# Kernel tuning notes

Hardware: AMD Instinct MI355X
Metric: run time of the kernel (lower is better)

The kernel has to match this reference:

```python
import jax, jax.numpy as jnp
import numpy as np

B, N, HIST, PRED = 32, 1500, 24, 24
OUT, FDIM = 1, 31
IN = OUT + FDIM          # 32 = chebconv in_dim
HID, GCN, K, E = 256, 256, 3, 24000


def setup_inputs() -> dict:
    key = jax.random.key(0)
    ks = jax.random.split(key, 8)
    x_hist = jax.random.normal(ks[0], (B, HIST, N, OUT), jnp.float32)
    features = jax.random.normal(ks[1], (B, HIST + PRED, N, FDIM), jnp.float32)
    edge_index = jax.random.randint(ks[2], (2, E), 0, N, dtype=jnp.int32)
    s_cheb = 1.0 / np.sqrt(IN)
    s_ih = 1.0 / np.sqrt(HID)
    W_cheb = jax.random.normal(ks[3], (K, IN, GCN), jnp.float32) * s_cheb
    b_cheb = jnp.zeros((GCN,), jnp.float32)
    W_ih = jax.random.normal(ks[4], (3 * HID, IN + GCN), jnp.float32) * s_ih
    b_ih = jnp.zeros((3 * HID,), jnp.float32)
    W_hh = jax.random.normal(ks[5], (3 * HID, HID), jnp.float32) * s_ih
    b_hh = jnp.zeros((3 * HID,), jnp.float32)
    W_fc = jax.random.normal(ks[6], (OUT, HID), jnp.float32) * s_ih
    b_fc = jnp.zeros((OUT,), jnp.float32)
    return dict(x_hist=x_hist, features=features, edge_index=edge_index,
                W_cheb=W_cheb, b_cheb=b_cheb, W_ih=W_ih, b_ih=b_ih,
                W_hh=W_hh, b_hh=b_hh, W_fc=W_fc, b_fc=b_fc)


def _edge_norm(edge_index):
    # sym-normalized Laplacian scaled by 2/lambda_max with lambda_max=2:
    # L_hat = -D^{-1/2} A D^{-1/2} (zero diagonal)
    src, dst = edge_index[0], edge_index[1]
    deg = jax.ops.segment_sum(jnp.ones((E,), jnp.float32), src, num_segments=N)
    dis = jnp.where(deg > 0, jax.lax.rsqrt(jnp.maximum(deg, 1.0)), 0.0)
    w = -(dis[src] * dis[dst])
    return src, dst, w


def _cheb(x, src, dst, w, W_cheb, b_cheb):
    # x: [B, N, D]; Chebyshev recursion Tx_k = 2 L_hat Tx_{k-1} - Tx_{k-2}
    def Lx(v):
        msg = v[:, src, :] * w[None, :, None]          # [B, E, D]
        return jnp.zeros_like(v).at[:, dst, :].add(msg)
    Tx0 = x
    out = jnp.einsum('bnd,df->bnf', Tx0, W_cheb[0])
    Tx1 = Lx(x)
    out = out + jnp.einsum('bnd,df->bnf', Tx1, W_cheb[1])
    for k in range(2, W_cheb.shape[0]):
        Tx2 = 2.0 * Lx(Tx1) - Tx0
        out = out + jnp.einsum('bnd,df->bnf', Tx2, W_cheb[k])
        Tx0, Tx1 = Tx1, Tx2
    return out + b_cheb


def _gru(x, h, W_ih, b_ih, W_hh, b_hh):
    # x: [B*N, IN+GCN], h: [B*N, HID]; torch.nn.GRUCell math
    gi = x @ W_ih.T + b_ih
    gh = h @ W_hh.T + b_hh
    i_r, i_z, i_n = jnp.split(gi, 3, axis=-1)
    h_r, h_z, h_n = jnp.split(gh, 3, axis=-1)
    r = jax.nn.sigmoid(i_r + h_r)
    z = jax.nn.sigmoid(i_z + h_z)
    n = jnp.tanh(i_n + r * h_n)
    return (1.0 - z) * n + z * h


def reference(x_hist, features, edge_index, W_cheb, b_cheb, W_ih, b_ih, W_hh, b_hh, W_fc, b_fc):
    src, dst, w = _edge_norm(edge_index)

    def step(h, x_t):
        g = jax.nn.sigmoid(_cheb(x_t, src, dst, w, W_cheb, b_cheb))   # [B,N,GCN]
        xg = jnp.concatenate([x_t, g], axis=-1).reshape(B * N, IN + GCN)
        return _gru(xg, h, W_ih, b_ih, W_hh, b_hh)

    # encoder: t = 1 .. hist_len-1, x_t = [x_hist[:,t-1], features[:,t]]
    xs = jnp.concatenate([x_hist[:, :HIST - 1], features[:, 1:HIST]], axis=-1)
    xs = jnp.moveaxis(xs, 1, 0)                                       # [HIST-1,B,N,IN]
    h0 = jnp.zeros((B * N, HID), x_hist.dtype)
    hn, _ = jax.lax.scan(lambda h, x_t: (step(h, x_t), None), h0, xs)

    feats_dec = jnp.moveaxis(features[:, HIST:], 1, 0)                # [PRED,B,N,FDIM]

    def dec_step(carry, f_t):
        h, x_prev = carry
        x_t = jnp.concatenate([x_prev, f_t], axis=-1)                 # [B,N,IN]
        h = step(h, x_t)
        x_new = h.reshape(B, N, HID) @ W_fc.T + b_fc                  # [B,N,OUT]
        return (h, x_new), x_new

    (_, _), ys = jax.lax.scan(dec_step, (hn, x_hist[:, -1]), feats_dec)
    return jnp.moveaxis(ys, 0, 1)                                     # [B,PRED,N,OUT]
```

## Files before the change

kernel.cpp:

```cpp
#include <hip/hip_runtime.h>
#include <hip/hip_bf16.h>
#include <math.h>

#define NB 32
#define NN 1500
#define NE 24000
#define HIST_L 24
#define PRED_L 24
#define FDIM 31
#define INUM 32
#define HID 256
#define ROWS (NB*NN)
#define XGW 320
#define CTXW 96
#define NRB 375

typedef float f32x4 __attribute__((ext_vector_type(4)));
typedef short bf16x8 __attribute__((ext_vector_type(8)));
typedef short bf16x4 __attribute__((ext_vector_type(4)));

__device__ __forceinline__ float sigf(float x){ return 1.0f/(1.0f+expf(-x)); }
__device__ __forceinline__ unsigned short f2b(float f){
    __hip_bfloat16 h = __float2bfloat16(f);
    return __builtin_bit_cast(unsigned short, h);
}
__device__ __forceinline__ float b2f(unsigned short u){
    unsigned int x = ((unsigned int)u) << 16;
    return __builtin_bit_cast(float, x);
}

#define AS1 __attribute__((address_space(1)))
#define AS3 __attribute__((address_space(3)))
__device__ __forceinline__ void gload16(const void* g, void* l){
    __builtin_amdgcn_global_load_lds((const AS1 unsigned int*)g, (AS3 unsigned int*)l, 16, 0, 0);
}

__global__ void k_count(const int* __restrict__ ei, int* deg, int* cnt){
    int e = blockIdx.x*blockDim.x + threadIdx.x;
    if (e < NE){ atomicAdd(&deg[ei[e]], 1); atomicAdd(&cnt[ei[NE+e]], 1); }
}

__global__ void k_prefix(const int* __restrict__ cnt, int* __restrict__ coff){
    int lane = threadIdx.x;
    const int CH = (NN + 63)/64;
    int s = 0;
    for (int i=0;i<CH;i++){ int n = lane*CH+i; if (n<NN) s += cnt[n]; }
    int incl = s;
    for (int off=1; off<64; off<<=1){ int v = __shfl_up(incl, off); if (lane>=off) incl += v; }
    int run = incl - s;
    for (int i=0;i<CH;i++){ int n = lane*CH+i; if (n<NN){ coff[n] = run; run += cnt[n]; } }
    if (lane==63) coff[NN] = run;
}

__global__ __launch_bounds__(256) void k_fillw(
    const int* __restrict__ ei, const int* __restrict__ deg,
    const int* __restrict__ coff, int* __restrict__ csrc, float* __restrict__ cw){
    int n = blockIdx.x*4 + (threadIdx.x >> 6);
    if (n >= NN) return;
    int lane = threadIdx.x & 63;
    int dn = deg[n];
    float disn = dn>0 ? rsqrtf((float)dn) : 0.0f;
    int pos = coff[n];
    for (int base=0; base<NE; base+=64){
        int e = base + lane;
        int d = ei[NE+e];
        bool m = (d == n);
        unsigned long long mask = __ballot(m);
        if (m){
            int rank = __popcll(mask & ((1ull<<lane)-1ull));
            int s = ei[e];
            int ds = deg[s];
            float diss = ds>0 ? rsqrtf((float)ds) : 0.0f;
            csrc[pos+rank] = s;
            cw[pos+rank] = -(diss*disn);
        }
        pos += __popcll(mask);
    }
}

__global__ void k_f2b(const float* __restrict__ src, unsigned short* __restrict__ dst, int n){
    int i = blockIdx.x*256 + threadIdx.x;
    if (i < n) dst[i] = f2b(src[i]);
}
__global__ void k_wihr(const float* __restrict__ W, unsigned short* __restrict__ Wr){
    int i = blockIdx.x*256 + threadIdx.x;
    if (i < 768*XGW){
        int r = i/XGW, c = i - r*XGW;
        Wr[i] = (c < INUM+HID) ? f2b(W[(size_t)r*(INUM+HID) + c]) : (unsigned short)0;
    }
}
__global__ void k_wctr(const float* __restrict__ Wc, unsigned short* __restrict__ W){
    int i = blockIdx.x*256 + threadIdx.x;
    if (i < 256*96){
        int j = i/96, k = i - j*96;
        W[i] = f2b(Wc[(size_t)k*256 + j]);
    }
}

__global__ void k_build(const float* __restrict__ ch0, int bstride, int choff0, int chstep, int addb,
                        const float* __restrict__ bfc,
                        const float* __restrict__ feats, int tf0,
                        float* __restrict__ xt, unsigned short* __restrict__ ctx,
                        unsigned short* __restrict__ xg){
    int s = blockIdx.y;
    int idx = blockIdx.x*blockDim.x + threadIdx.x;
    if (idx >= ROWS*INUM) return;
    xt  += (size_t)s*ROWS*INUM;
    ctx += (size_t)s*ROWS*CTXW;
    xg  += (size_t)s*ROWS*XGW;
    int choff = choff0 + s*chstep;
    int tf = tf0 + s;
    int r = idx >> 5, c = idx & 31;
    int b = r / NN, n = r - b*NN;
    float v;
    if (c == 0){ v = ch0[b*bstride + choff + n]; if (addb) v += bfc[0]; }
    else         v = feats[((size_t)(b*(HIST_L+PRED_L) + tf)*NN + n)*FDIM + (c-1)];
    xt[idx] = v;
    unsigned short bv = f2b(v);
    ctx[(size_t)r*CTXW + c] = bv;
    xg[(size_t)r*XGW + c] = bv;
}

__global__ void k_lx4(const float* __restrict__ vin, const int* __restrict__ coff,
                      const int* __restrict__ csrc, const float* __restrict__ cw,
                      const float* __restrict__ sub, float scale,
                      float* __restrict__ vout, unsigned short* __restrict__ ctxo){
    int s = blockIdx.y;
    int idx = blockIdx.x*256 + threadIdx.x;
    if (idx >= ROWS*8) return;
    vin += (size_t)s*ROWS*INUM;
    if (sub)  sub  += (size_t)s*ROWS*INUM;
    if (vout) vout += (size_t)s*ROWS*INUM;
    ctxo += (size_t)s*ROWS*CTXW;
    int r = idx >> 3, l8 = idx & 7;
    int b = r / NN, n = r - b*NN;
    int j0 = coff[n], j1 = coff[n+1];
    const float4* vb = (const float4*)(vin + (size_t)b*NN*INUM);
    float ax=0.f, ay=0.f, az=0.f, aw=0.f;
    for (int j=j0;j<j1;j++){
        float w = cw[j];
        float4 v = vb[csrc[j]*8 + l8];
        ax += w*v.x; ay += w*v.y; az += w*v.z; aw += w*v.w;
    }
    ax *= scale; ay *= scale; az *= scale; aw *= scale;
    if (sub){
        float4 sv = ((const float4*)sub)[idx];
        ax -= sv.x; ay -= sv.y; az -= sv.z; aw -= sv.w;
    }
    if (vout){
        float4 o; o.x=ax; o.y=ay; o.z=az; o.w=aw;
        ((float4*)vout)[idx] = o;
    }
    bf16x4 ob;
    ob[0]=(short)f2b(ax); ob[1]=(short)f2b(ay); ob[2]=(short)f2b(az); ob[3]=(short)f2b(aw);
    *(bf16x4*)&ctxo[(size_t)r*CTXW + l8*4] = ob;
}

__global__ __launch_bounds__(256,2) void k_cheb3(
    const unsigned short* __restrict__ ctx, const unsigned short* __restrict__ Wctr,
    const float* __restrict__ bc, unsigned short* __restrict__ xg)
{
    __shared__ __align__(16) unsigned short A[128*104];
    __shared__ __align__(16) unsigned short B[256*104];
    const int bi = blockIdx.x;
    const int s = bi / NRB, rb = bi - s*NRB;
    ctx += (size_t)s*ROWS*CTXW;
    xg  += (size_t)s*ROWS*XGW;
    const int tid = threadIdx.x, wid = tid>>6, lane = tid&63;
    const int wm = wid>>1, wn = wid&1;
    const int r0 = rb*128;
    const int l15 = lane&15, lhi = lane>>4;

    #pragma unroll
    for (int i=0;i<6;i++){
        int idx = tid + i*256;
        int row = idx/12, c = idx - row*12;
        *(int4*)&A[row*104 + c*8] = *(const int4*)&ctx[(size_t)(r0+row)*96 + c*8];
    }
    #pragma unroll
    for (int i=0;i<12;i++){
        int idx = tid + i*256;
        int row = idx/12, c = idx - row*12;
        *(int4*)&B[row*104 + c*8] = *(const int4*)&Wctr[(size_t)row*96 + c*8];
    }
    __syncthreads();

    f32x4 acc[4][8] = {};
    #pragma unroll
    for (int ks=0; ks<3; ks++){
        bf16x8 a[4];
        #pragma unroll
        for (int mi=0;mi<4;mi++)
            a[mi] = *(const bf16x8*)&A[(wm*64+mi*16+l15)*104 + ks*32 + lhi*8];
        #pragma unroll
        for (int ni=0;ni<8;ni++){
            bf16x8 b = *(const bf16x8*)&B[(wn*128+ni*16+l15)*104 + ks*32 + lhi*8];
            #pragma unroll
            for (int mi=0;mi<4;mi++)
                acc[mi][ni] = __builtin_amdgcn_mfma_f32_16x16x32_bf16(a[mi], b, acc[mi][ni],0,0,0);
        }
    }
    #pragma unroll
    for (int ni=0;ni<8;ni++){
        int col = wn*128 + ni*16 + l15;
        float bcv = bc[col];
        #pragma unroll
        for (int mi=0;mi<4;mi++){
            #pragma unroll
            for (int v=0;v<4;v++){
                size_t row = r0 + wm*64 + mi*16 + lhi*4 + v;
                xg[row*XGW + 32 + col] = f2b(sigf(acc[mi][ni][v] + bcv));
            }
        }
    }
}

__device__ __forceinline__ void gtile32(const unsigned short* Ap, const unsigned short* Bp,
    int wm, int wn, int l15, int q,
    f32x4 (&ar)[4][2], f32x4 (&az)[4][2], f32x4 (&a3)[4][2])
{
    bf16x8 a[4];
    #pragma unroll
    for (int mi=0;mi<4;mi++)
        a[mi] = *(const bf16x8*)&Ap[(wm*64 + mi*16 + l15)*32 + q];
    #pragma unroll
    for (int slab=0; slab<3; slab++){
        bf16x8 b0 = *(const bf16x8*)&Bp[(slab*64 + wn*32 + l15)*32 + q];
        bf16x8 b1 = *(const bf16x8*)&Bp[(slab*64 + wn*32 + 16 + l15)*32 + q];
        f32x4 (&acc)[4][2] = (slab==0)?ar:((slab==1)?az:a3);
        #pragma unroll
        for (int mi=0;mi<4;mi++){
            acc[mi][0] = __builtin_amdgcn_mfma_f32_16x16x32_bf16(a[mi], b0, acc[mi][0],0,0,0);
            acc[mi][1] = __builtin_amdgcn_mfma_f32_16x16x32_bf16(a[mi], b1, acc[mi][1],0,0,0);
        }
    }
}

__global__ __launch_bounds__(256,2) void k_gru6(
    const unsigned short* __restrict__ xg, const unsigned short* __restrict__ hbin,
    const unsigned short* __restrict__ Wihr, const unsigned short* __restrict__ Whhr,
    const float* __restrict__ bih, const float* __restrict__ bhh,
    unsigned short* __restrict__ hbout,
    const float* __restrict__ Wfc, float* __restrict__ outp, int p)
{
    __shared__ __align__(16) unsigned short As[2][128*32];
    __shared__ __align__(16) unsigned short Bs[2][192*32];
    const int bi = blockIdx.x;
    const int xc = bi & 7, t = bi >> 3;
    const int R = xc + 8*(t>>2);
    if (R >= NRB) return;
    const int r0 = R*128, j0 = (t&3)*64;

    const int tid = threadIdx.x, wid = tid>>6, lane = tid&63;
    const int wm = wid>>1, wn = wid&1;
    const int l15 = lane&15, lhi = lane>>4;
    const int r4 = lane>>2;
    const int swz = ((lane&3) ^ ((lane>>3)&3))*16;
    const int q   = (lhi ^ ((l15>>1)&3))*8;

    f32x4 ar[4][2]={}, az[4][2]={}, ain[4][2]={}, ahn[4][2]={};

    auto stageA = [&](int ks, int bs){
        const char* src; size_t stride;
        if (ks < 9){ src = (const char*)xg   + (size_t)r0*640 + (size_t)ks*64;     stride = 640; }
        else       { src = (const char*)hbin + (size_t)r0*512 + (size_t)(ks-9)*64; stride = 512; }
        char* Ld = (char*)&As[bs][0] + wid*2048;
        #pragma unroll
        for (int i=0;i<2;i++){
            int lrow = wid*32 + i*16 + r4;
            gload16(src + (size_t)lrow*stride + swz, Ld + i*1024);
        }
    };
    auto stageB = [&](int ks, int bs){
        const char* src; size_t stride; int kb;
        if (ks < 9){ src = (const char*)Wihr; stride = 640; kb = ks; }
        else       { src = (const char*)Whhr; stride = 512; kb = ks-9; }
        src += (size_t)kb*64 + swz;
        char* Ld = (char*)&Bs[bs][0] + wid*3072;
        #pragma unroll
        for (int i=0;i<3;i++){
            int j = wid*3 + i;
            int wrow = (j>>2)*256 + j0 + (j&3)*16 + r4;
            gload16(src + (size_t)wrow*stride, Ld + i*1024);
        }
    };

    stageA(0,0); stageB(0,0);
    __syncthreads();
    for (int ks=0; ks<9; ks++){
        int cur = ks&1;
        { stageA(ks+1, cur^1); stageB(ks+1, cur^1); }
        gtile32(&As[cur][0], &Bs[cur][0], wm, wn, l15, q, ar, az, ain);
        __syncthreads();
    }
    for (int ks=9; ks<17; ks++){
        int cur = ks&1;
        if (ks<16){ stageA(ks+1, cur^1); stageB(ks+1, cur^1); }
        gtile32(&As[cur][0], &Bs[cur][0], wm, wn, l15, q, ar, az, ahn);
        __syncthreads();
    }
    float fcp[4][4] = {};
    float wf[2];
    if (p >= 0){
        wf[0] = Wfc[j0 + wn*32 + l15];
        wf[1] = Wfc[j0 + wn*32 + 16 + l15];
    }
    #pragma unroll
    for (int ni=0; ni<2; ni++){
        int col = j0 + wn*32 + ni*16 + l15;
        float br = bih[col]       + bhh[col];
        float bz = bih[col+HID]   + bhh[col+HID];
        float bi2 = bih[col+2*HID];
        float bh = bhh[col+2*HID];
        #pragma unroll
        for (int mi=0; mi<4; mi++){
            #pragma unroll
            for (int v=0; v<4; v++){
                size_t row = r0 + wm*64 + mi*16 + lhi*4 + v;
                float r  = sigf(ar[mi][ni][v] + br);
                float z  = sigf(az[mi][ni][v] + bz);
                float nn = tanhf(ain[mi][ni][v] + bi2 + r*(ahn[mi][ni][v] + bh));
                float ho = b2f(hbin[row*HID + col]);
                float hv = (1.f - z)*nn + z*ho;
                hbout[row*HID + col] = f2b(hv);
                if (p >= 0) fcp[mi][v] += hv * wf[ni];
            }
        }
    }
    if (p >= 0){
        #pragma unroll
        for (int mi=0; mi<4; mi++){
            #pragma unroll
            for (int v=0; v<4; v++){
                float s = fcp[mi][v];
                s += __shfl_xor(s, 1);
                s += __shfl_xor(s, 2);
                s += __shfl_xor(s, 4);
                s += __shfl_xor(s, 8);
                if (l15 == 0){
                    int row = r0 + wm*64 + mi*16 + lhi*4 + v;
                    int bb = row / NN, n = row - bb*NN;
                    atomicAdd(&outp[(size_t)(bb*PRED_L + p)*NN + n], s);
                }
            }
        }
    }
}

extern "C" void kernel_launch(void* const* d_in, const int* in_sizes, int n_in,
                              void* d_out, int out_size, void* d_ws, size_t ws_size,
                              hipStream_t stream){
    const float* x_hist = (const float*)d_in[0];
    const float* feats  = (const float*)d_in[1];
    const int*   ei     = (const int*)d_in[2];
    const float* Wc     = (const float*)d_in[3];
    const float* bc     = (const float*)d_in[4];
    const float* Wih    = (const float*)d_in[5];
    const float* bih    = (const float*)d_in[6];
    const float* Whh    = (const float*)d_in[7];
    const float* bhh    = (const float*)d_in[8];
    const float* Wfc    = (const float*)d_in[9];
    const float* bfc    = (const float*)d_in[10];
    float* out = (float*)d_out;

    char* wsp = (char*)d_ws;
    size_t off = 0;
    auto alloc = [&](size_t bytes)->char*{
        char* p = wsp + off; off = (off + bytes + 255) & ~(size_t)255; return p;
    };
    int*   deg  = (int*)  alloc(NN*4);
    int*   cnt  = (int*)  alloc(NN*4);
    int*   coff = (int*)  alloc((NN+1)*4);
    int*   csrc = (int*)  alloc(NE*4);
    float* cw   = (float*)alloc(NE*4);
    unsigned short* hbA = (unsigned short*)alloc((size_t)ROWS*HID*2);
    unsigned short* hbB = (unsigned short*)alloc((size_t)ROWS*HID*2);
    unsigned short* Wihr = (unsigned short*)alloc((size_t)768*XGW*2);
    unsigned short* Whhr = (unsigned short*)alloc((size_t)768*HID*2);
    unsigned short* Wctr = (unsigned short*)alloc((size_t)256*CTXW*2);

    const size_t perSlice = (size_t)ROWS*INUM*4*2 + (size_t)ROWS*CTXW*2 + (size_t)ROWS*XGW*2 + 4*256;
    int CH = 1;
    for (int c : {8,6,4,2}){
        if (off + (size_t)c*perSlice + (1<<20) <= ws_size){ CH = c; break; }
    }
    float* xt_b = (float*)alloc((size_t)CH*ROWS*INUM*4);
    float* T1_b = (float*)alloc((size_t)CH*ROWS*INUM*4);
    unsigned short* ctx_b = (unsigned short*)alloc((size_t)CH*ROWS*CTXW*2);
    unsigned short* xg_b  = (unsigned short*)alloc((size_t)CH*ROWS*XGW*2);

    hipMemsetAsync(deg, 0, NN*4, stream);
    hipMemsetAsync(cnt, 0, NN*4, stream);
    hipMemsetAsync(hbA, 0, (size_t)ROWS*HID*2, stream);
    hipMemsetAsync(xg_b, 0, (size_t)CH*ROWS*XGW*2, stream);
    hipMemsetAsync(out, 0, (size_t)out_size*4, stream);

    k_count<<<(NE+255)/256,256,0,stream>>>(ei, deg, cnt);
    k_prefix<<<1,64,0,stream>>>(cnt, coff);
    k_fillw<<<NRB,256,0,stream>>>(ei, deg, coff, csrc, cw);

    { int n = 768*XGW; k_wihr<<<(n+255)/256,256,0,stream>>>(Wih, Wihr); }
    { int n = 768*HID; k_f2b<<<(n+255)/256,256,0,stream>>>(Whh, Whhr, n); }
    { int n = 256*CTXW; k_wctr<<<(n+255)/256,256,0,stream>>>(Wc, Wctr); }

    unsigned short* hbin = hbA; unsigned short* hbout = hbB;
    const int gruGrid = 1504;
    const int NT  = (ROWS*INUM+255)/256;
    const int NT8 = (ROWS*8+255)/256;

    for (int t0=0; t0<HIST_L-1; t0+=CH){
        int nc = HIST_L-1-t0; if (nc > CH) nc = CH;
        dim3 gb(NT, nc), gl(NT8, nc);
        k_build<<<gb,256,0,stream>>>(x_hist, HIST_L*NN, t0*NN, NN, 0, bfc, feats, t0+1, xt_b, ctx_b, xg_b);
        k_lx4<<<gl,256,0,stream>>>(xt_b, coff, csrc, cw, nullptr, 1.f, T1_b, ctx_b + 32);
        k_lx4<<<gl,256,0,stream>>>(T1_b, coff, csrc, cw, xt_b, 2.f, nullptr, ctx_b + 64);
        k_cheb3<<<NRB*nc,256,0,stream>>>(ctx_b, Wctr, bc, xg_b);
        for (int s=0; s<nc; s++){
            k_gru6<<<gruGrid,256,0,stream>>>(xg_b + (size_t)s*ROWS*XGW, hbin, Wihr, Whhr, bih, bhh, hbout, Wfc, out, -1);
            unsigned short* tmp = hbin; hbin = hbout; hbout = tmp;
        }
    }
    for (int p=0;p<PRED_L;p++){
        dim3 gb(NT,1), gl(NT8,1);
        if (p==0) k_build<<<gb,256,0,stream>>>(x_hist, HIST_L*NN, (HIST_L-1)*NN, 0, 0, bfc, feats, HIST_L+p, xt_b, ctx_b, xg_b);
        else      k_build<<<gb,256,0,stream>>>(out, PRED_L*NN, (p-1)*NN, 0, 1, bfc, feats, HIST_L+p, xt_b, ctx_b, xg_b);
        k_lx4<<<gl,256,0,stream>>>(xt_b, coff, csrc, cw, nullptr, 1.f, T1_b, ctx_b + 32);
        k_lx4<<<gl,256,0,stream>>>(T1_b, coff, csrc, cw, xt_b, 2.f, nullptr, ctx_b + 64);
        k_cheb3<<<NRB,256,0,stream>>>(ctx_b, Wctr, bc, xg_b);
        k_gru6<<<gruGrid,256,0,stream>>>(xg_b, hbin, Wihr, Whhr, bih, bhh, hbout, Wfc, out, p);
        unsigned short* tmp = hbin; hbin = hbout; hbout = tmp;
    }
}
```

Baseline: 6.928 ms.

## Fuse recurrent GRU and decoder steps into one persistent cooperative kernel

The encoder's Chebyshev inputs for all 23 timesteps are now precomputed in chunks into one large xg buffer. A single cooperative persistent kernel then runs every encoder GRU step and every full decoder step, with grid.sync between phases. The GRU, Chebyshev matmul and graph-propagation phases become grid-stride device functions sharing one static LDS block. This aims to remove about 150 kernel launches and their gaps, in exchange for grid-wide barrier costs, a much larger workspace, and a GRU tile order that loses the previous L2-friendly block swizzle.

```diff
diff --git a/kernel.cpp b/kernel.cpp
--- a/kernel.cpp
+++ b/kernel.cpp
@@ -1,6 +1,9 @@
 #include <hip/hip_runtime.h>
 #include <hip/hip_bf16.h>
+#include <hip/hip_cooperative_groups.h>
 #include <math.h>
+
+namespace cg = cooperative_groups;
 
 #define NB 32
 #define NN 1500
@@ -236,21 +239,13 @@
     }
 }
 
-__global__ __launch_bounds__(256,2) void k_gru6(
+__device__ __forceinline__ void gru_phase(char* smem,
     const unsigned short* __restrict__ xg, const unsigned short* __restrict__ hbin,
+    unsigned short* __restrict__ hbout,
     const unsigned short* __restrict__ Wihr, const unsigned short* __restrict__ Whhr,
     const float* __restrict__ bih, const float* __restrict__ bhh,
-    unsigned short* __restrict__ hbout,
     const float* __restrict__ Wfc, float* __restrict__ outp, int p)
 {
-    __shared__ __align__(16) unsigned short As[2][128*32];
-    __shared__ __align__(16) unsigned short Bs[2][192*32];
-    const int bi = blockIdx.x;
-    const int xc = bi & 7, t = bi >> 3;
-    const int R = xc + 8*(t>>2);
-    if (R >= NRB) return;
-    const int r0 = R*128, j0 = (t&3)*64;
-
     const int tid = threadIdx.x, wid = tid>>6, lane = tid&63;
     const int wm = wid>>1, wn = wid&1;
     const int l15 = lane&15, lhi = lane>>4;
@@ -258,92 +253,237 @@
     const int swz = ((lane&3) ^ ((lane>>3)&3))*16;
     const int q   = (lhi ^ ((l15>>1)&3))*8;
 
-    f32x4 ar[4][2]={}, az[4][2]={}, ain[4][2]={}, ahn[4][2]={};
-
-    auto stageA = [&](int ks, int bs){
-        const char* src; size_t stride;
-        if (ks < 9){ src = (const char*)xg   + (size_t)r0*640 + (size_t)ks*64;     stride = 640; }
-        else       { src = (const char*)hbin + (size_t)r0*512 + (size_t)(ks-9)*64; stride = 512; }
-        char* Ld = (char*)&As[bs][0] + wid*2048;
-        #pragma unroll
-        for (int i=0;i<2;i++){
-            int lrow = wid*32 + i*16 + r4;
-            gload16(src + (size_t)lrow*stride + swz, Ld + i*1024);
-        }
-    };
-    auto stageB = [&](int ks, int bs){
-        const char* src; size_t stride; int kb;
-        if (ks < 9){ src = (const char*)Wihr; stride = 640; kb = ks; }
-        else       { src = (const char*)Whhr; stride = 512; kb = ks-9; }
-        src += (size_t)kb*64 + swz;
-        char* Ld = (char*)&Bs[bs][0] + wid*3072;
-        #pragma unroll
-        for (int i=0;i<3;i++){
-            int j = wid*3 + i;
-            int wrow = (j>>2)*256 + j0 + (j&3)*16 + r4;
-            gload16(src + (size_t)wrow*stride, Ld + i*1024);
-        }
-    };
-
-    stageA(0,0); stageB(0,0);
-    __syncthreads();
-    for (int ks=0; ks<9; ks++){
-        int cur = ks&1;
-        { stageA(ks+1, cur^1); stageB(ks+1, cur^1); }
-        gtile32(&As[cur][0], &Bs[cur][0], wm, wn, l15, q, ar, az, ain);
+    for (int job = blockIdx.x; job < NRB*4; job += gridDim.x){
+        const int r0 = (job>>2)*128, j0 = (job&3)*64;
+        f32x4 ar[4][2]={}, az[4][2]={}, ain[4][2]={}, ahn[4][2]={};
+
+        auto stageA = [&](int ks, int bs){
+            const char* src; size_t stride;
+            if (ks < 9){ src = (const char*)xg   + (size_t)r0*640 + (size_t)ks*64;     stride = 640; }
+            else       { src = (const char*)hbin + (size_t)r0*512 + (size_t)(ks-9)*64; stride = 512; }
+            char* Ld = smem + bs*8192 + wid*2048;
+            #pragma unroll
+            for (int i=0;i<2;i++){
+                int lrow = wid*32 + i*16 + r4;
+                gload16(src + (size_t)lrow*stride + swz, Ld + i*1024);
+            }
+        };
+        auto stageB = [&](int ks, int bs){
+            const char* src; size_t stride; int kb;
+            if (ks < 9){ src = (const char*)Wihr; stride = 640; kb = ks; }
+            else       { src = (const char*)Whhr; stride = 512; kb = ks-9; }
+            src += (size_t)kb*64 + swz;
+            char* Ld = smem + 16384 + bs*12288 + wid*3072;
+            #pragma unroll
+            for (int i=0;i<3;i++){
+                int j = wid*3 + i;
+                int wrow = (j>>2)*256 + j0 + (j&3)*16 + r4;
+                gload16(src + (size_t)wrow*stride, Ld + i*1024);
+            }
+        };
+
+        stageA(0,0); stageB(0,0);
         __syncthreads();
-    }
-    for (int ks=9; ks<17; ks++){
-        int cur = ks&1;
-        if (ks<16){ stageA(ks+1, cur^1); stageB(ks+1, cur^1); }
-        gtile32(&As[cur][0], &Bs[cur][0], wm, wn, l15, q, ar, az, ahn);
+        for (int ks=0; ks<9; ks++){
+            int cur = ks&1;
+            stageA(ks+1, cur^1); stageB(ks+1, cur^1);
+            gtile32((const unsigned short*)(smem + cur*8192),
+                    (const unsigned short*)(smem + 16384 + cur*12288), wm, wn, l15, q, ar, az, ain);
+            __syncthreads();
+        }
+        for (int ks=9; ks<17; ks++){
+            int cur = ks&1;
+            if (ks<16){ stageA(ks+1, cur^1); stageB(ks+1, cur^1); }
+            gtile32((const unsigned short*)(smem + cur*8192),
+                    (const unsigned short*)(smem + 16384 + cur*12288), wm, wn, l15, q, ar, az, ahn);
+            __syncthreads();
+        }
+        float fcp[4][4] = {};
+        float wf[2];
+        if (p >= 0){
+            wf[0] = Wfc[j0 + wn*32 + l15];
+            wf[1] = Wfc[j0 + wn*32 + 16 + l15];
+        }
+        #pragma unroll
+        for (int ni=0; ni<2; ni++){
+            int col = j0 + wn*32 + ni*16 + l15;
+            float br = bih[col]       + bhh[col];
+            float bz = bih[col+HID]   + bhh[col+HID];
+            float bi2 = bih[col+2*HID];
+            float bh = bhh[col+2*HID];
+            #pragma unroll
+            for (int mi=0; mi<4; mi++){
+                #pragma unroll
+                for (int v=0; v<4; v++){
+                    size_t row = r0 + wm*64 + mi*16 + lhi*4 + v;
+                    float r  = sigf(ar[mi][ni][v] + br);
+                    float z  = sigf(az[mi][ni][v] + bz);
+                    float nn = tanhf(ain[mi][ni][v] + bi2 + r*(ahn[mi][ni][v] + bh));
+                    float ho = b2f(hbin[row*HID + col]);
+                    float hv = (1.f - z)*nn + z*ho;
+                    hbout[row*HID + col] = f2b(hv);
+                    if (p >= 0) fcp[mi][v] += hv * wf[ni];
+                }
+            }
+        }
+        if (p >= 0){
+            #pragma unroll
+            for (int mi=0; mi<4; mi++){
+                #pragma unroll
+                for (int v=0; v<4; v++){
+                    float s = fcp[mi][v];
+                    s += __shfl_xor(s, 1);
+                    s += __shfl_xor(s, 2);
+                    s += __shfl_xor(s, 4);
+                    s += __shfl_xor(s, 8);
+                    if (l15 == 0){
+                        int row = r0 + wm*64 + mi*16 + lhi*4 + v;
+                        int bb = row / NN, n = row - bb*NN;
+                        atomicAdd(&outp[(size_t)(bb*PRED_L + p)*NN + n], s);
+                    }
+                }
+            }
+        }
+    }
+}
+
+__device__ __forceinline__ void cheb_phase(char* smem,
+    const unsigned short* __restrict__ ctx, const unsigned short* __restrict__ Wctr,
+    const float* __restrict__ bc, unsigned short* __restrict__ xg)
+{
+    unsigned short* A = (unsigned short*)smem;
+    unsigned short* B = (unsigned short*)(smem + 26624);
+    const int tid = threadIdx.x, wid = tid>>6, lane = tid&63;
+    const int wm = wid>>1, wn = wid&1;
+    const int l15 = lane&15, lhi = lane>>4;
+    for (int jb = blockIdx.x; jb < NRB; jb += gridDim.x){
+        const int r0 = jb*128;
+        #pragma unroll
+        for (int i=0;i<6;i++){
+            int idx = tid + i*256;
+            int row = idx/12, c = idx - row*12;
+            *(int4*)&A[row*104 + c*8] = *(const int4*)&ctx[(size_t)(r0+row)*96 + c*8];
+        }
+        #pragma unroll
+        for (int i=0;i<12;i++){
+            int idx = tid + i*256;
+            int row = idx/12, c = idx - row*12;
+            *(int4*)&B[row*104 + c*8] = *(const int4*)&Wctr[(size_t)row*96 + c*8];
+        }
         __syncthreads();
-    }
-    float fcp[4][4] = {};
-    float wf[2];
-    if (p >= 0){
-        wf[0] = Wfc[j0 + wn*32 + l15];
-        wf[1] = Wfc[j0 + wn*32 + 16 + l15];
-    }
-    #pragma unroll
-    for (int ni=0; ni<2; ni++){
-        int col = j0 + wn*32 + ni*16 + l15;
-        float br = bih[col]       + bhh[col];
-        float bz = bih[col+HID]   + bhh[col+HID];
-        float bi2 = bih[col+2*HID];
-        float bh = bhh[col+2*HID];
-        #pragma unroll
-        for (int mi=0; mi<4; mi++){
-            #pragma unroll
-            for (int v=0; v<4; v++){
-                size_t row = r0 + wm*64 + mi*16 + lhi*4 + v;
-                float r  = sigf(ar[mi][ni][v] + br);
-                float z  = sigf(az[mi][ni][v] + bz);
-                float nn = tanhf(ain[mi][ni][v] + bi2 + r*(ahn[mi][ni][v] + bh));
-                float ho = b2f(hbin[row*HID + col]);
-                float hv = (1.f - z)*nn + z*ho;
-                hbout[row*HID + col] = f2b(hv);
-                if (p >= 0) fcp[mi][v] += hv * wf[ni];
-            }
-        }
-    }
-    if (p >= 0){
-        #pragma unroll
-        for (int mi=0; mi<4; mi++){
-            #pragma unroll
-            for (int v=0; v<4; v++){
-                float s = fcp[mi][v];
-                s += __shfl_xor(s, 1);
-                s += __shfl_xor(s, 2);
-                s += __shfl_xor(s, 4);
-                s += __shfl_xor(s, 8);
-                if (l15 == 0){
-                    int row = r0 + wm*64 + mi*16 + lhi*4 + v;
-                    int bb = row / NN, n = row - bb*NN;
-                    atomicAdd(&outp[(size_t)(bb*PRED_L + p)*NN + n], s);
+        f32x4 acc[4][8] = {};
+        #pragma unroll
+        for (int ks=0; ks<3; ks++){
+            bf16x8 a[4];
+            #pragma unroll
+            for (int mi=0;mi<4;mi++)
+                a[mi] = *(const bf16x8*)&A[(wm*64+mi*16+l15)*104 + ks*32 + lhi*8];
+            #pragma unroll
+            for (int ni=0;ni<8;ni++){
+                bf16x8 b = *(const bf16x8*)&B[(wn*128+ni*16+l15)*104 + ks*32 + lhi*8];
+                #pragma unroll
+                for (int mi=0;mi<4;mi++)
+                    acc[mi][ni] = __builtin_amdgcn_mfma_f32_16x16x32_bf16(a[mi], b, acc[mi][ni],0,0,0);
+            }
+        }
+        #pragma unroll
+        for (int ni=0;ni<8;ni++){
+            int col = wn*128 + ni*16 + l15;
+            float bcv = bc[col];
+            #pragma unroll
+            for (int mi=0;mi<4;mi++){
+                #pragma unroll
+                for (int v=0;v<4;v++){
+                    size_t row = r0 + wm*64 + mi*16 + lhi*4 + v;
+                    xg[row*XGW + 32 + col] = f2b(sigf(acc[mi][ni][v] + bcv));
                 }
             }
         }
+        __syncthreads();
+    }
+}
+
+__device__ __forceinline__ void lx_phase(
+    const float* __restrict__ vin, const int* __restrict__ coff,
+    const int* __restrict__ csrc, const float* __restrict__ cw,
+    const float* __restrict__ sub, float scale,
+    float* __restrict__ vout, unsigned short* __restrict__ ctxo)
+{
+    const int stride = gridDim.x*blockDim.x;
+    for (int idx = blockIdx.x*blockDim.x + threadIdx.x; idx < ROWS*8; idx += stride){
+        int r = idx >> 3, l8 = idx & 7;
+        int b = r / NN, n = r - b*NN;
+        int j0 = coff[n], j1 = coff[n+1];
+        const float4* vb = (const float4*)(vin + (size_t)b*NN*INUM);
+        float ax=0.f, ay=0.f, az=0.f, aw=0.f;
+        for (int j=j0;j<j1;j++){
+            float w = cw[j];
+            float4 v = vb[csrc[j]*8 + l8];
+            ax += w*v.x; ay += w*v.y; az += w*v.z; aw += w*v.w;
+        }
+        ax *= scale; ay *= scale; az *= scale; aw *= scale;
+        if (sub){
+            float4 sv = ((const float4*)sub)[idx];
+            ax -= sv.x; ay -= sv.y; az -= sv.z; aw -= sv.w;
+        }
+        if (vout){
+            float4 o; o.x=ax; o.y=ay; o.z=az; o.w=aw;
+            ((float4*)vout)[idx] = o;
+        }
+        bf16x4 ob;
+        ob[0]=(short)f2b(ax); ob[1]=(short)f2b(ay); ob[2]=(short)f2b(az); ob[3]=(short)f2b(aw);
+        *(bf16x4*)&ctxo[(size_t)r*CTXW + l8*4] = ob;
+    }
+}
+
+__global__ __launch_bounds__(256,2) void k_recur(
+    unsigned short* xg_b, float* xt, float* T1, unsigned short* ctx,
+    unsigned short* hbA, unsigned short* hbB,
+    const unsigned short* Wihr, const unsigned short* Whhr, const unsigned short* Wctr,
+    const float* bih, const float* bhh, const float* bc, const float* bfc,
+    const float* Wfc, const float* x_hist, const float* feats,
+    const int* coff, const int* csrc, const float* cw, float* out)
+{
+    cg::grid_group grid = cg::this_grid();
+    __shared__ __align__(16) char smem[79872];
+    unsigned short* hbin = hbA;
+    unsigned short* hbout = hbB;
+    const int gstride = gridDim.x*blockDim.x;
+
+    for (int t=0; t<HIST_L-1; ++t){
+        gru_phase(smem, xg_b + (size_t)t*ROWS*XGW, hbin, hbout, Wihr, Whhr, bih, bhh, Wfc, out, -1);
+        { unsigned short* tmp=hbin; hbin=hbout; hbout=tmp; }
+        grid.sync();
+    }
+    for (int p=0; p<PRED_L; ++p){
+        {
+            const float* ch0 = (p==0)? x_hist : out;
+            const int bstride = (p==0)? HIST_L*NN : PRED_L*NN;
+            const int choff = (p==0)? (HIST_L-1)*NN : (p-1)*NN;
+            const int addb = (p==0)? 0 : 1;
+            const int tf = HIST_L + p;
+            for (int idx = blockIdx.x*blockDim.x + threadIdx.x; idx < ROWS*INUM; idx += gstride){
+                int r = idx >> 5, c = idx & 31;
+                int b = r / NN, n = r - b*NN;
+                float v;
+                if (c == 0){ v = ch0[b*bstride + choff + n]; if (addb) v += bfc[0]; }
+                else         v = feats[((size_t)(b*(HIST_L+PRED_L) + tf)*NN + n)*FDIM + (c-1)];
+                xt[idx] = v;
+                unsigned short bv = f2b(v);
+                ctx[(size_t)r*CTXW + c] = bv;
+                xg_b[(size_t)r*XGW + c] = bv;
+            }
+        }
+        grid.sync();
+        lx_phase(xt, coff, csrc, cw, nullptr, 1.f, T1, ctx + 32);
+        grid.sync();
+        lx_phase(T1, coff, csrc, cw, xt, 2.f, nullptr, ctx + 64);
+        grid.sync();
+        cheb_phase(smem, ctx, Wctr, bc, xg_b);
+        grid.sync();
+        gru_phase(smem, xg_b, hbin, hbout, Wihr, Whhr, bih, bhh, Wfc, out, p);
+        { unsigned short* tmp=hbin; hbin=hbout; hbout=tmp; }
+        grid.sync();
     }
 }
 
@@ -379,7 +519,9 @@
     unsigned short* Whhr = (unsigned short*)alloc((size_t)768*HID*2);
     unsigned short* Wctr = (unsigned short*)alloc((size_t)256*CTXW*2);
 
-    const size_t perSlice = (size_t)ROWS*INUM*4*2 + (size_t)ROWS*CTXW*2 + (size_t)ROWS*XGW*2 + 4*256;
+    unsigned short* xg_b = (unsigned short*)alloc((size_t)(HIST_L-1)*ROWS*XGW*2);
+
+    const size_t perSlice = (size_t)ROWS*INUM*4*2 + (size_t)ROWS*CTXW*2 + 4*256;
     int CH = 1;
     for (int c : {8,6,4,2}){
         if (off + (size_t)c*perSlice + (1<<20) <= ws_size){ CH = c; break; }
@@ -387,12 +529,11 @@
     float* xt_b = (float*)alloc((size_t)CH*ROWS*INUM*4);
     float* T1_b = (float*)alloc((size_t)CH*ROWS*INUM*4);
     unsigned short* ctx_b = (unsigned short*)alloc((size_t)CH*ROWS*CTXW*2);
-    unsigned short* xg_b  = (unsigned short*)alloc((size_t)CH*ROWS*XGW*2);
 
     hipMemsetAsync(deg, 0, NN*4, stream);
     hipMemsetAsync(cnt, 0, NN*4, stream);
     hipMemsetAsync(hbA, 0, (size_t)ROWS*HID*2, stream);
-    hipMemsetAsync(xg_b, 0, (size_t)CH*ROWS*XGW*2, stream);
+    hipMemsetAsync(xg_b, 0, (size_t)(HIST_L-1)*ROWS*XGW*2, stream);
     hipMemsetAsync(out, 0, (size_t)out_size*4, stream);
 
     k_count<<<(NE+255)/256,256,0,stream>>>(ei, deg, cnt);
@@ -403,31 +544,32 @@
     { int n = 768*HID; k_f2b<<<(n+255)/256,256,0,stream>>>(Whh, Whhr, n); }
     { int n = 256*CTXW; k_wctr<<<(n+255)/256,256,0,stream>>>(Wc, Wctr); }
 
-    unsigned short* hbin = hbA; unsigned short* hbout = hbB;
-    const int gruGrid = 1504;
     const int NT  = (ROWS*INUM+255)/256;
     const int NT8 = (ROWS*8+255)/256;
 
     for (int t0=0; t0<HIST_L-1; t0+=CH){
         int nc = HIST_L-1-t0; if (nc > CH) nc = CH;
         dim3 gb(NT, nc), gl(NT8, nc);
-        k_build<<<gb,256,0,stream>>>(x_hist, HIST_L*NN, t0*NN, NN, 0, bfc, feats, t0+1, xt_b, ctx_b, xg_b);
+        unsigned short* xg_t = xg_b + (size_t)t0*ROWS*XGW;
+        k_build<<<gb,256,0,stream>>>(x_hist, HIST_L*NN, t0*NN, NN, 0, bfc, feats, t0+1, xt_b, ctx_b, xg_t);
         k_lx4<<<gl,256,0,stream>>>(xt_b, coff, csrc, cw, nullptr, 1.f, T1_b, ctx_b + 32);
         k_lx4<<<gl,256,0,stream>>>(T1_b, coff, csrc, cw, xt_b, 2.f, nullptr, ctx_b + 64);
-        k_cheb3<<<NRB*nc,256,0,stream>>>(ctx_b, Wctr, bc, xg_b);
-        for (int s=0; s<nc; s++){
-            k_gru6<<<gruGrid,256,0,stream>>>(xg_b + (size_t)s*ROWS*XGW, hbin, Wihr, Whhr, bih, bhh, hbout, Wfc, out, -1);
-            unsigned short* tmp = hbin; hbin = hbout; hbout = tmp;
-        }
-    }
-    for (int p=0;p<PRED_L;p++){
-        dim3 gb(NT,1), gl(NT8,1);
-        if (p==0) k_build<<<gb,256,0,stream>>>(x_hist, HIST_L*NN, (HIST_L-1)*NN, 0, 0, bfc, feats, HIST_L+p, xt_b, ctx_b, xg_b);
-        else      k_build<<<gb,256,0,stream>>>(out, PRED_L*NN, (p-1)*NN, 0, 1, bfc, feats, HIST_L+p, xt_b, ctx_b, xg_b);
-        k_lx4<<<gl,256,0,stream>>>(xt_b, coff, csrc, cw, nullptr, 1.f, T1_b, ctx_b + 32);
-        k_lx4<<<gl,256,0,stream>>>(T1_b, coff, csrc, cw, xt_b, 2.f, nullptr, ctx_b + 64);
-        k_cheb3<<<NRB,256,0,stream>>>(ctx_b, Wctr, bc, xg_b);
-        k_gru6<<<gruGrid,256,0,stream>>>(xg_b, hbin, Wihr, Whhr, bih, bhh, hbout, Wfc, out, p);
-        unsigned short* tmp = hbin; hbin = hbout; hbout = tmp;
-    }
-}
+        k_cheb3<<<NRB*nc,256,0,stream>>>(ctx_b, Wctr, bc, xg_t);
+    }
+
+    int maxb = 0;
+    if (hipOccupancyMaxActiveBlocksPerMultiprocessor(&maxb, (const void*)k_recur, 256, 0) != hipSuccess || maxb < 1)
+        maxb = 2;
+    int grid = maxb * 256;
+    if (grid > 1024) grid = 1024;
+
+    void* args[] = {
+        (void*)&xg_b, (void*)&xt_b, (void*)&T1_b, (void*)&ctx_b,
+        (void*)&hbA, (void*)&hbB,
+        (void*)&Wihr, (void*)&Whhr, (void*)&Wctr,
+        (void*)&bih, (void*)&bhh, (void*)&bc, (void*)&bfc,
+        (void*)&Wfc, (void*)&x_hist, (void*)&feats,
+        (void*)&coff, (void*)&csrc, (void*)&cw, (void*)&out
+    };
+    hipLaunchCooperativeKernel((const void*)k_recur, dim3(grid), dim3(256), args, 0, stream);
+}
```

New measurement: 19.05 ms. 2.75x slower.
